# Kernel optimization log

Hardware: AMD Instinct MI355X
Metric: run time of the kernel (lower is better)

Reference implementation:

```python
import jax, jax.numpy as jnp
import numpy as np
import math

STRIDES = [8, 16, 32, 64, 128]
NUM_CLASSES = 80
NUM_ANCHORS = 9
_RATIOS = np.array([0.5, 1.0, 2.0])
_SCALES = 2.0 ** np.array([0.0, 1.0 / 3.0, 2.0 / 3.0])


def _base_anchors(base_size):
    # standard RetinaNet base anchors: 3 ratios x 3 scales, centered at origin
    a = np.zeros((9, 4))
    a[:, 2:] = base_size * np.tile(_SCALES, (2, 3)).T
    areas = a[:, 2] * a[:, 3]
    a[:, 2] = np.sqrt(areas / np.repeat(_RATIOS, 3))
    a[:, 3] = a[:, 2] * np.repeat(_RATIOS, 3)
    a[:, 0::2] -= np.tile(a[:, 2] * 0.5, (2, 1)).T
    a[:, 1::2] -= np.tile(a[:, 3] * 0.5, (2, 1)).T
    return a


def _make_anchors(featmap_sizes):
    per_level = []
    for (h, w), s in zip(featmap_sizes, STRIDES):
        base = _base_anchors(4 * s)  # base_size = 4 * stride (RetinaNet convention)
        sx = (np.arange(w) + 0.5) * s
        sy = (np.arange(h) + 0.5) * s
        X, Y = np.meshgrid(sx, sy)
        shifts = np.stack([X.ravel(), Y.ravel(), X.ravel(), Y.ravel()], axis=1)
        # anchors vary fastest per location -> matches [B,H,W,A,*] flatten order
        per_level.append((shifts[:, None, :] + base[None, :, :]).reshape(-1, 4))
    return jnp.asarray(np.concatenate(per_level, axis=0), dtype=jnp.float32)


def _conv3x3(x, w, b):
    y = jax.lax.conv_general_dilated(x, w, (1, 1), 'SAME', dimension_numbers=('NCHW', 'OIHW', 'NCHW'))
    return y + b[None, :, None, None]


def _tower(x, ws, bs):
    for i in range(4):
        x = jax.nn.relu(_conv3x3(x, ws[i], bs[i]))
    return _conv3x3(x, ws[4], bs[4])


def _bbox_transform(anchors, deltas):
    # BBoxTransform with mean 0, std (0.1, 0.1, 0.2, 0.2)
    w = anchors[:, 2] - anchors[:, 0]
    h = anchors[:, 3] - anchors[:, 1]
    cx = anchors[:, 0] + 0.5 * w
    cy = anchors[:, 1] + 0.5 * h
    pcx = cx + deltas[..., 0] * 0.1 * w
    pcy = cy + deltas[..., 1] * 0.1 * h
    pw = jnp.exp(deltas[..., 2] * 0.2) * w
    ph = jnp.exp(deltas[..., 3] * 0.2) * h
    return jnp.stack([pcx - 0.5 * pw, pcy - 0.5 * ph, pcx + 0.5 * pw, pcy + 0.5 * ph], axis=-1)


def _heads(feats, cls_ws, cls_bs, reg_ws, reg_bs):
    B = feats[0].shape[0]
    cls_l, reg_l = [], []
    for f in feats:
        c = _tower(f, cls_ws, cls_bs)  # [B, 9*80, H, W]
        cls_l.append(jnp.transpose(c, (0, 2, 3, 1)).reshape(B, -1, NUM_CLASSES))
        r = _tower(f, reg_ws, reg_bs)  # [B, 9*4, H, W]
        reg_l.append(jnp.transpose(r, (0, 2, 3, 1)).reshape(B, -1, 4))
    return jnp.concatenate(cls_l, axis=1), jnp.concatenate(reg_l, axis=1)


def setup_inputs():
    key = jax.random.key(0)
    ks = jax.random.split(key, 32)
    B, C = 8, 256
    sizes = [(64, 64), (32, 32), (16, 16), (8, 8), (4, 4)]
    inp = {}
    for i, (h, w) in enumerate(sizes):
        inp['feat%d' % i] = jax.random.normal(ks[i], (B, C, h, w), dtype=jnp.float32)
    prior_bias = -math.log((1.0 - 0.01) / 0.01)

    def mk(k, out_ch, in_ch):
        std = math.sqrt(2.0 / (9.0 * out_ch))  # matches torch init normal_(0, sqrt(2/n))
        return jax.random.normal(k, (out_ch, in_ch, 3, 3), dtype=jnp.float32) * std

    ki = 5
    for i in range(4):
        inp['cls_w%d' % i] = mk(ks[ki], 256, 256); ki += 1
        inp['cls_b%d' % i] = jnp.zeros((256,), jnp.float32)
    inp['cls_w4'] = mk(ks[ki], NUM_ANCHORS * NUM_CLASSES, 256); ki += 1
    inp['cls_b4'] = jnp.full((NUM_ANCHORS * NUM_CLASSES,), prior_bias, jnp.float32)
    for i in range(4):
        inp['reg_w%d' % i] = mk(ks[ki], 256, 256); ki += 1
        inp['reg_b%d' % i] = jnp.zeros((256,), jnp.float32)
    inp['reg_w4'] = mk(ks[ki], NUM_ANCHORS * 4, 256); ki += 1
    inp['reg_b4'] = jnp.full((NUM_ANCHORS * 4,), prior_bias, jnp.float32)
    return inp


def reference(feat0, feat1, feat2, feat3, feat4,
              cls_w0, cls_b0, cls_w1, cls_b1, cls_w2, cls_b2, cls_w3, cls_b3, cls_w4, cls_b4,
              reg_w0, reg_b0, reg_w1, reg_b1, reg_w2, reg_b2, reg_w3, reg_b3, reg_w4, reg_b4):
    feats = [feat0, feat1, feat2, feat3, feat4]
    cls_ws = [cls_w0, cls_w1, cls_w2, cls_w3, cls_w4]
    cls_bs = [cls_b0, cls_b1, cls_b2, cls_b3, cls_b4]
    reg_ws = [reg_w0, reg_w1, reg_w2, reg_w3, reg_w4]
    reg_bs = [reg_b0, reg_b1, reg_b2, reg_b3, reg_b4]
    pred_cls, pred_reg = _heads(feats, cls_ws, cls_bs, reg_ws, reg_bs)
    anchors = _make_anchors([f.shape[-2:] for f in feats])  # [A, 4]
    boxes = _bbox_transform(anchors, pred_reg)  # [B, A, 4]
    probs = jax.nn.sigmoid(pred_cls)  # [B, A, 80]
    scores = jnp.max(probs, axis=2)
    class_id = jnp.argmax(probs, axis=2)
    return scores, class_id, boxes
```

## Files before the change

kernel.cpp:

```cpp
#include <hip/hip_runtime.h>
#include <math.h>

#define CIN 256
#define K9  2304
#define TLW 16
#define TLH 8
#define LIS 22
#define TAU 1e-3f

template<typename TI, typename TA, int CH, bool RELU>
__global__ __launch_bounds__(256, 2) void conv_tile(
    const TI* __restrict__ in, const float* __restrict__ wgt,
    const float* __restrict__ bias, TA* __restrict__ out,
    int H, int W, int C_out)
{
    const int NCH = CIN / CH;
    const int tilesX = (W + TLW - 1) / TLW;
    const int tx = (blockIdx.x % tilesX) * TLW;
    const int ty = (blockIdx.x / tilesX) * TLH;
    const int b  = blockIdx.y;
    const int co0 = blockIdx.z * 64;
    const int tid = threadIdx.x;
    const int tco = (tid >> 5) * 8;
    const int tpx = tid & 31;
    const int prow = tpx >> 2;
    const int pcol = (tpx & 3) * 4;

    __shared__ __align__(16) TA lw[CH * 9 * 64];
    __shared__ __align__(16) TA li[CH * 10 * LIS];

    TA acc[8][4];
    #pragma unroll
    for (int c = 0; c < 8; ++c)
        #pragma unroll
        for (int j = 0; j < 4; ++j) acc[c][j] = (TA)0;

    const int coLim = min(64, C_out - co0);

    for (int ch = 0; ch < NCH; ++ch) {
        const int ci0 = ch * CH;
        for (int idx = tid; idx < CH * 9 * 64; idx += 256) {
            int r  = idx >> 6;
            int co = idx & 63;
            TA v = (TA)0;
            if (co < coLim)
                v = (TA)wgt[(size_t)(co0 + co) * (CIN * 9) + (size_t)ci0 * 9 + r];
            lw[idx] = v;
        }
        for (int idx = tid; idx < CH * 10 * LIS; idx += 256) {
            int ci = idx / (10 * LIS);
            int rr = idx % (10 * LIS);
            int row = rr / LIS, col = rr % LIS;
            TA v = (TA)0;
            int iy = ty + row - 1, ix = tx + col - 1;
            if (col < TLW + 2 && iy >= 0 && iy < H && ix >= 0 && ix < W)
                v = (TA)in[(((size_t)b * CIN + ci0 + ci) * H + iy) * W + ix];
            li[idx] = v;
        }
        __syncthreads();
        #pragma unroll
        for (int ci = 0; ci < CH; ++ci) {
            #pragma unroll
            for (int ky = 0; ky < 3; ++ky) {
                const TA* ip = &li[ci * 10 * LIS + (prow + ky) * LIS + pcol];
                TA ir[6];
                #pragma unroll
                for (int t = 0; t < 6; ++t) ir[t] = ip[t];
                #pragma unroll
                for (int kx = 0; kx < 3; ++kx) {
                    const TA* wp = &lw[(ci * 9 + ky * 3 + kx) * 64 + tco];
                    TA wv[8];
                    #pragma unroll
                    for (int c = 0; c < 8; ++c) wv[c] = wp[c];
                    TA x0 = ir[kx], x1 = ir[kx + 1], x2 = ir[kx + 2], x3 = ir[kx + 3];
                    #pragma unroll
                    for (int c = 0; c < 8; ++c) {
                        acc[c][0] += wv[c] * x0;
                        acc[c][1] += wv[c] * x1;
                        acc[c][2] += wv[c] * x2;
                        acc[c][3] += wv[c] * x3;
                    }
                }
            }
        }
        __syncthreads();
    }

    const int oy = ty + prow;
    if (oy < H) {
        #pragma unroll
        for (int c = 0; c < 8; ++c) {
            int co = co0 + tco + c;
            if (co < C_out) {
                TA bv = (TA)bias[co];
                #pragma unroll
                for (int j = 0; j < 4; ++j) {
                    int ox = tx + pcol + j;
                    if (ox < W) {
                        TA v = acc[c][j] + bv;
                        if (RELU) v = v > (TA)0 ? v : (TA)0;
                        out[(((size_t)b * C_out + co) * H + oy) * W + ox] = v;
                    }
                }
            }
        }
    }
}

#define CH5 8
__global__ __launch_bounds__(256, 2) void cls5_f32(
    const double* __restrict__ in, const float* __restrict__ wgt,
    const float* __restrict__ bias, float* __restrict__ scores,
    float* __restrict__ cls_id, unsigned char* __restrict__ flags,
    int H, int W, int level_off, int A_total, int b0)
{
    const int tilesX = (W + TLW - 1) / TLW;
    const int tx = (blockIdx.x % tilesX) * TLW;
    const int ty = (blockIdx.x / tilesX) * TLH;
    const int b  = blockIdx.y;
    const int a  = blockIdx.z;
    const int co0 = a * 80;
    const int tid = threadIdx.x;
    const int cog = tid >> 5;
    const int tco = cog * 10;
    const int tpx = tid & 31;
    const int prow = tpx >> 2;
    const int pcol = (tpx & 3) * 4;

    __shared__ __align__(16) float lw[CH5 * 9 * 80];
    __shared__ __align__(16) float li[CH5 * 10 * LIS];
    __shared__ float redM1[128 * 8];
    __shared__ float redM2[128 * 8];
    __shared__ int   redA [128 * 8];

    float acc[10][4];
    #pragma unroll
    for (int c = 0; c < 10; ++c)
        #pragma unroll
        for (int j = 0; j < 4; ++j) acc[c][j] = 0.f;

    for (int ch = 0; ch < CIN / CH5; ++ch) {
        const int ci0 = ch * CH5;
        for (int idx = tid; idx < CH5 * 9 * 80; idx += 256) {
            int r  = idx / 80;
            int co = idx % 80;
            lw[idx] = wgt[(size_t)(co0 + co) * (CIN * 9) + (size_t)ci0 * 9 + r];
        }
        for (int idx = tid; idx < CH5 * 10 * LIS; idx += 256) {
            int ci = idx / (10 * LIS);
            int rr = idx % (10 * LIS);
            int row = rr / LIS, col = rr % LIS;
            float v = 0.f;
            int iy = ty + row - 1, ix = tx + col - 1;
            if (col < TLW + 2 && iy >= 0 && iy < H && ix >= 0 && ix < W)
                v = (float)in[(((size_t)b * CIN + ci0 + ci) * H + iy) * W + ix];
            li[idx] = v;
        }
        __syncthreads();
        #pragma unroll
        for (int ci = 0; ci < CH5; ++ci) {
            #pragma unroll
            for (int ky = 0; ky < 3; ++ky) {
                const float* ip = &li[ci * 10 * LIS + (prow + ky) * LIS + pcol];
                float ir[6];
                #pragma unroll
                for (int t = 0; t < 6; ++t) ir[t] = ip[t];
                #pragma unroll
                for (int kx = 0; kx < 3; ++kx) {
                    const float* wp = &lw[(ci * 9 + ky * 3 + kx) * 80 + tco];
                    float wv[10];
                    #pragma unroll
                    for (int c = 0; c < 10; ++c) wv[c] = wp[c];
                    float x0 = ir[kx], x1 = ir[kx + 1], x2 = ir[kx + 2], x3 = ir[kx + 3];
                    #pragma unroll
                    for (int c = 0; c < 10; ++c) {
                        acc[c][0] = fmaf(wv[c], x0, acc[c][0]);
                        acc[c][1] = fmaf(wv[c], x1, acc[c][1]);
                        acc[c][2] = fmaf(wv[c], x2, acc[c][2]);
                        acc[c][3] = fmaf(wv[c], x3, acc[c][3]);
                    }
                }
            }
        }
        __syncthreads();
    }

    #pragma unroll
    for (int j = 0; j < 4; ++j) {
        float m1 = acc[0][j] + bias[co0 + tco];
        float m2 = -3.0e38f;
        int am = tco;
        #pragma unroll
        for (int c = 1; c < 10; ++c) {
            float v = acc[c][j] + bias[co0 + tco + c];
            if (v > m1) { m2 = m1; m1 = v; am = tco + c; }
            else if (v > m2) { m2 = v; }
        }
        int p = prow * 16 + pcol + j;
        redM1[p * 8 + cog] = m1;
        redA [p * 8 + cog] = am;
        redM2[p * 8 + cog] = m2;
    }
    __syncthreads();
    if (tid < 128) {
        int p = tid;
        float m1 = redM1[p * 8]; int am = redA[p * 8]; float m2 = redM2[p * 8];
        #pragma unroll
        for (int t = 1; t < 8; ++t) {
            float rm1 = redM1[p * 8 + t];
            float rm2 = redM2[p * 8 + t];
            if (rm1 > m1) { m2 = fmaxf(m1, rm2); m1 = rm1; am = redA[p * 8 + t]; }
            else          { m2 = fmaxf(m2, rm1); }
        }
        int oy = ty + (p >> 4), ox = tx + (p & 15);
        if (oy < H && ox < W) {
            size_t oi = (size_t)(b0 + b) * A_total + level_off
                      + (size_t)(oy * W + ox) * 9 + a;
            scores[oi] = 1.f / (1.f + expf(-m1));
            cls_id[oi] = (float)am;
            flags[((size_t)b * H * W + oy * W + ox) * 9 + a] =
                (m1 - m2 < TAU) ? 1 : 0;
        }
    }
}

__global__ __launch_bounds__(128) void fixup_cls(
    const double* __restrict__ in, const float* __restrict__ wgt,
    const float* __restrict__ bias, const unsigned char* __restrict__ flags,
    float* __restrict__ scores, float* __restrict__ cls_id,
    int H, int W, int level_off, int A_total, int b0)
{
    const int px = blockIdx.x;
    const int b  = blockIdx.y;
    const int a  = blockIdx.z;
    const int tid = threadIdx.x;
    const unsigned char fl = flags[((size_t)b * H * W + px) * 9 + a];

    __shared__ double patch[K9];
    __shared__ double lg[80];

    if (fl) {
        const int y = px / W, x = px % W;
        for (int idx = tid; idx < K9; idx += 128) {
            int ci = idx / 9, tap = idx % 9;
            int iy = y + tap / 3 - 1, ix = x + tap % 3 - 1;
            double v = 0.0;
            if (iy >= 0 && iy < H && ix >= 0 && ix < W)
                v = in[(((size_t)b * CIN + ci) * H + iy) * W + ix];
            patch[idx] = v;
        }
        __syncthreads();
        if (tid < 80) {
            const float* wr = wgt + (size_t)(a * 80 + tid) * K9;
            double s = 0.0;
            for (int k = 0; k < K9; ++k) s += (double)wr[k] * patch[k];
            lg[tid] = s + (double)bias[a * 80 + tid];
        }
        __syncthreads();
        if (tid == 0) {
            double m = lg[0]; int am = 0;
            for (int c = 1; c < 80; ++c)
                if (lg[c] > m) { m = lg[c]; am = c; }
            size_t oi = (size_t)(b0 + b) * A_total + level_off + (size_t)px * 9 + a;
            scores[oi] = (float)(1.0 / (1.0 + exp(-m)));
            cls_id[oi] = (float)am;
        }
    }
}

__global__ void boxes_ep(const float* __restrict__ reg5, float* __restrict__ boxes,
                         int H, int W, int level_off, int A_total, float stride,
                         int b0, int Bc)
{
    int idx = blockIdx.x * 256 + threadIdx.x;
    int total = Bc * H * W * 9;
    if (idx >= total) return;
    int a = idx % 9; int rest = idx / 9;
    int x = rest % W; rest /= W;
    int y = rest % H; int b = rest / H;

    float base = 4.f * stride;
    float scale = exp2f((float)(a % 3) * (1.f / 3.f));
    int ri = a / 3;
    float sr = (ri == 0) ? 0.70710678118654752f : (ri == 1 ? 1.f : 1.41421356237309505f);
    float wa = base * scale / sr;
    float ha = base * scale * sr;
    float cx = (x + 0.5f) * stride, cy = (y + 0.5f) * stride;

    size_t cs = (size_t)H * W;
    const float* rp = reg5 + (((size_t)b * 36 + a * 4) * H + y) * W + x;
    float d0 = rp[0], d1 = rp[cs], d2 = rp[2 * cs], d3 = rp[3 * cs];

    float pcx = cx + d0 * 0.1f * wa;
    float pcy = cy + d1 * 0.1f * ha;
    float pw  = expf(d2 * 0.2f) * wa;
    float ph  = expf(d3 * 0.2f) * ha;

    size_t oi = ((size_t)(b0 + b) * A_total + level_off
               + (size_t)(y * W + x) * 9 + a) * 4;
    boxes[oi + 0] = pcx - 0.5f * pw;
    boxes[oi + 1] = pcy - 0.5f * ph;
    boxes[oi + 2] = pcx + 0.5f * pw;
    boxes[oi + 3] = pcy + 0.5f * ph;
}

extern "C" void kernel_launch(void* const* d_in, const int* in_sizes, int n_in,
                              void* d_out, int out_size, void* d_ws, size_t ws_size,
                              hipStream_t stream)
{
    const float* feats[5];
    for (int i = 0; i < 5; ++i) feats[i] = (const float*)d_in[i];
    const float* cw[5]; const float* cb[5];
    const float* rw[5]; const float* rb[5];
    for (int i = 0; i < 5; ++i) {
        cw[i] = (const float*)d_in[5 + 2 * i];
        cb[i] = (const float*)d_in[6 + 2 * i];
        rw[i] = (const float*)d_in[15 + 2 * i];
        rb[i] = (const float*)d_in[16 + 2 * i];
    }

    const int A_total = 49104;
    float* scores = (float*)d_out;
    float* cls_id = scores + (size_t)8 * A_total;
    float* boxes  = scores + (size_t)2 * 8 * A_total;

    const int   Hs[5]      = {64, 32, 16, 8, 4};
    const float strides[5] = {8.f, 16.f, 32.f, 64.f, 128.f};
    const int   offs[5]    = {0, 36864, 46080, 48384, 48960};

    const size_t flagRes = 131072;
    unsigned char* flags = (unsigned char*)d_ws;
    char*  actBase  = (char*)d_ws + flagRes;
    size_t actBytes = ws_size > flagRes ? ws_size - flagRes : 0;

    for (int l = 0; l < 5; ++l) {
        int H = Hs[l], W = Hs[l];
        size_t perb = (size_t)CIN * H * W;
        int Bc = 8;
        while (Bc > 1 && 2ull * Bc * perb * 8 > actBytes) Bc >>= 1;
        double* D0 = (double*)actBase;
        double* D1 = D0 + (size_t)Bc * perb;
        int tiles = ((W + TLW - 1) / TLW) * ((H + TLH - 1) / TLH);
        for (int b0 = 0; b0 < 8; b0 += Bc) {
            const float* fin = feats[l] + (size_t)b0 * perb;
            dim3 g(tiles, Bc, 4);
            conv_tile<float,  double, 8, true><<<g, 256, 0, stream>>>(fin, cw[0], cb[0], D0, H, W, 256);
            conv_tile<double, double, 8, true><<<g, 256, 0, stream>>>(D0,  cw[1], cb[1], D1, H, W, 256);
            conv_tile<double, double, 8, true><<<g, 256, 0, stream>>>(D1,  cw[2], cb[2], D0, H, W, 256);
            conv_tile<double, double, 8, true><<<g, 256, 0, stream>>>(D0,  cw[3], cb[3], D1, H, W, 256);
            dim3 g5(tiles, Bc, 9);
            cls5_f32<<<g5, 256, 0, stream>>>(D1, cw[4], cb[4], scores, cls_id,
                                             flags, H, W, offs[l], A_total, b0);
            dim3 gf(H * W, Bc, 9);
            fixup_cls<<<gf, 128, 0, stream>>>(D1, cw[4], cb[4], flags,
                                              scores, cls_id,
                                              H, W, offs[l], A_total, b0);
        }
    }

    for (int l = 0; l < 5; ++l) {
        int H = Hs[l], W = Hs[l];
        size_t perb = (size_t)CIN * H * W;
        int Br = 8;
        while (Br > 1 && 2ull * Br * perb * 4 > actBytes) Br >>= 1;
        float* F0 = (float*)actBase;
        float* F1 = F0 + (size_t)Br * perb;
        int tiles = ((W + TLW - 1) / TLW) * ((H + TLH - 1) / TLH);
        for (int b0 = 0; b0 < 8; b0 += Br) {
            dim3 g(tiles, Br, 4);
            const float* fin = feats[l] + (size_t)b0 * perb;
            conv_tile<float, float, 8, true><<<g, 256, 0, stream>>>(fin, rw[0], rb[0], F0, H, W, 256);
            conv_tile<float, float, 8, true><<<g, 256, 0, stream>>>(F0,  rw[1], rb[1], F1, H, W, 256);
            conv_tile<float, float, 8, true><<<g, 256, 0, stream>>>(F1,  rw[2], rb[2], F0, H, W, 256);
            conv_tile<float, float, 8, true><<<g, 256, 0, stream>>>(F0,  rw[3], rb[3], F1, H, W, 256);
            dim3 gr(tiles, Br, 1);
            conv_tile<float, float, 8, false><<<gr, 256, 0, stream>>>(F1, rw[4], rb[4], F0, H, W, 36);
            int total = Br * H * W * 9;
            boxes_ep<<<(total + 255) / 256, 256, 0, stream>>>(F0, boxes, H, W,
                                                              offs[l], A_total,
                                                              strides[l], b0, Br);
        }
    }
}
```

Measured before the change: 24.80 ms.

## Unfuse final cls conv from argmax epilogue; reuse generic conv tile

Replaces the specialized fused final classification conv (conv plus per-tile max/argmax reduction through shared memory) with the generic conv_tile kernel writing the 720-channel logits to a float workspace. A separate elementwise epilogue kernel then computes the top-2, sigmoid score, class id and tie flag per anchor. This drops the shared-memory reduction and the 10-channel-per-thread register layout of the fused kernel in favour of the generic conv's 64-channel blocking. In exchange it adds a logits round trip through global memory and shrinks the batch chunk to fit the extra buffer.

```diff
diff --git a/kernel.cpp b/kernel.cpp
--- a/kernel.cpp
+++ b/kernel.cpp
@@ -107,120 +107,27 @@
     }
 }
 
-#define CH5 8
-__global__ __launch_bounds__(256, 2) void cls5_f32(
-    const double* __restrict__ in, const float* __restrict__ wgt,
-    const float* __restrict__ bias, float* __restrict__ scores,
+__global__ __launch_bounds__(256) void cls_ep(
+    const float* __restrict__ lg, float* __restrict__ scores,
     float* __restrict__ cls_id, unsigned char* __restrict__ flags,
-    int H, int W, int level_off, int A_total, int b0)
-{
-    const int tilesX = (W + TLW - 1) / TLW;
-    const int tx = (blockIdx.x % tilesX) * TLW;
-    const int ty = (blockIdx.x / tilesX) * TLH;
-    const int b  = blockIdx.y;
-    const int a  = blockIdx.z;
-    const int co0 = a * 80;
-    const int tid = threadIdx.x;
-    const int cog = tid >> 5;
-    const int tco = cog * 10;
-    const int tpx = tid & 31;
-    const int prow = tpx >> 2;
-    const int pcol = (tpx & 3) * 4;
-
-    __shared__ __align__(16) float lw[CH5 * 9 * 80];
-    __shared__ __align__(16) float li[CH5 * 10 * LIS];
-    __shared__ float redM1[128 * 8];
-    __shared__ float redM2[128 * 8];
-    __shared__ int   redA [128 * 8];
-
-    float acc[10][4];
-    #pragma unroll
-    for (int c = 0; c < 10; ++c)
-        #pragma unroll
-        for (int j = 0; j < 4; ++j) acc[c][j] = 0.f;
-
-    for (int ch = 0; ch < CIN / CH5; ++ch) {
-        const int ci0 = ch * CH5;
-        for (int idx = tid; idx < CH5 * 9 * 80; idx += 256) {
-            int r  = idx / 80;
-            int co = idx % 80;
-            lw[idx] = wgt[(size_t)(co0 + co) * (CIN * 9) + (size_t)ci0 * 9 + r];
-        }
-        for (int idx = tid; idx < CH5 * 10 * LIS; idx += 256) {
-            int ci = idx / (10 * LIS);
-            int rr = idx % (10 * LIS);
-            int row = rr / LIS, col = rr % LIS;
-            float v = 0.f;
-            int iy = ty + row - 1, ix = tx + col - 1;
-            if (col < TLW + 2 && iy >= 0 && iy < H && ix >= 0 && ix < W)
-                v = (float)in[(((size_t)b * CIN + ci0 + ci) * H + iy) * W + ix];
-            li[idx] = v;
-        }
-        __syncthreads();
-        #pragma unroll
-        for (int ci = 0; ci < CH5; ++ci) {
-            #pragma unroll
-            for (int ky = 0; ky < 3; ++ky) {
-                const float* ip = &li[ci * 10 * LIS + (prow + ky) * LIS + pcol];
-                float ir[6];
-                #pragma unroll
-                for (int t = 0; t < 6; ++t) ir[t] = ip[t];
-                #pragma unroll
-                for (int kx = 0; kx < 3; ++kx) {
-                    const float* wp = &lw[(ci * 9 + ky * 3 + kx) * 80 + tco];
-                    float wv[10];
-                    #pragma unroll
-                    for (int c = 0; c < 10; ++c) wv[c] = wp[c];
-                    float x0 = ir[kx], x1 = ir[kx + 1], x2 = ir[kx + 2], x3 = ir[kx + 3];
-                    #pragma unroll
-                    for (int c = 0; c < 10; ++c) {
-                        acc[c][0] = fmaf(wv[c], x0, acc[c][0]);
-                        acc[c][1] = fmaf(wv[c], x1, acc[c][1]);
-                        acc[c][2] = fmaf(wv[c], x2, acc[c][2]);
-                        acc[c][3] = fmaf(wv[c], x3, acc[c][3]);
-                    }
-                }
-            }
-        }
-        __syncthreads();
-    }
-
-    #pragma unroll
-    for (int j = 0; j < 4; ++j) {
-        float m1 = acc[0][j] + bias[co0 + tco];
-        float m2 = -3.0e38f;
-        int am = tco;
-        #pragma unroll
-        for (int c = 1; c < 10; ++c) {
-            float v = acc[c][j] + bias[co0 + tco + c];
-            if (v > m1) { m2 = m1; m1 = v; am = tco + c; }
+    int HW, int level_off, int A_total, int b0, int Bc)
+{
+    int idx = blockIdx.x * 256 + threadIdx.x;
+    if (idx >= Bc * HW) return;
+    int b = idx / HW, px = idx % HW;
+    const float* base = lg + (size_t)b * 720 * HW + px;
+    for (int a = 0; a < 9; ++a) {
+        float m1 = -3.0e38f, m2 = -3.0e38f;
+        int am = 0;
+        for (int c = 0; c < 80; ++c) {
+            float v = base[(size_t)(a * 80 + c) * HW];
+            if (v > m1) { m2 = m1; m1 = v; am = c; }
             else if (v > m2) { m2 = v; }
         }
-        int p = prow * 16 + pcol + j;
-        redM1[p * 8 + cog] = m1;
-        redA [p * 8 + cog] = am;
-        redM2[p * 8 + cog] = m2;
-    }
-    __syncthreads();
-    if (tid < 128) {
-        int p = tid;
-        float m1 = redM1[p * 8]; int am = redA[p * 8]; float m2 = redM2[p * 8];
-        #pragma unroll
-        for (int t = 1; t < 8; ++t) {
-            float rm1 = redM1[p * 8 + t];
-            float rm2 = redM2[p * 8 + t];
-            if (rm1 > m1) { m2 = fmaxf(m1, rm2); m1 = rm1; am = redA[p * 8 + t]; }
-            else          { m2 = fmaxf(m2, rm1); }
-        }
-        int oy = ty + (p >> 4), ox = tx + (p & 15);
-        if (oy < H && ox < W) {
-            size_t oi = (size_t)(b0 + b) * A_total + level_off
-                      + (size_t)(oy * W + ox) * 9 + a;
-            scores[oi] = 1.f / (1.f + expf(-m1));
-            cls_id[oi] = (float)am;
-            flags[((size_t)b * H * W + oy * W + ox) * 9 + a] =
-                (m1 - m2 < TAU) ? 1 : 0;
-        }
+        size_t oi = (size_t)(b0 + b) * A_total + level_off + (size_t)px * 9 + a;
+        scores[oi] = 1.f / (1.f + expf(-m1));
+        cls_id[oi] = (float)am;
+        flags[((size_t)b * HW + px) * 9 + a] = (m1 - m2 < TAU) ? 1 : 0;
     }
 }
 
@@ -335,11 +242,14 @@
 
     for (int l = 0; l < 5; ++l) {
         int H = Hs[l], W = Hs[l];
-        size_t perb = (size_t)CIN * H * W;
+        int HW = H * W;
+        size_t perb = (size_t)CIN * HW;
         int Bc = 8;
-        while (Bc > 1 && 2ull * Bc * perb * 8 > actBytes) Bc >>= 1;
+        while (Bc > 1 &&
+               (size_t)Bc * (16ull * perb + 2880ull * HW) > actBytes) Bc >>= 1;
         double* D0 = (double*)actBase;
         double* D1 = D0 + (size_t)Bc * perb;
+        float*  LG = (float*)(D1 + (size_t)Bc * perb);
         int tiles = ((W + TLW - 1) / TLW) * ((H + TLH - 1) / TLH);
         for (int b0 = 0; b0 < 8; b0 += Bc) {
             const float* fin = feats[l] + (size_t)b0 * perb;
@@ -348,10 +258,12 @@
             conv_tile<double, double, 8, true><<<g, 256, 0, stream>>>(D0,  cw[1], cb[1], D1, H, W, 256);
             conv_tile<double, double, 8, true><<<g, 256, 0, stream>>>(D1,  cw[2], cb[2], D0, H, W, 256);
             conv_tile<double, double, 8, true><<<g, 256, 0, stream>>>(D0,  cw[3], cb[3], D1, H, W, 256);
-            dim3 g5(tiles, Bc, 9);
-            cls5_f32<<<g5, 256, 0, stream>>>(D1, cw[4], cb[4], scores, cls_id,
-                                             flags, H, W, offs[l], A_total, b0);
-            dim3 gf(H * W, Bc, 9);
+            dim3 g5(tiles, Bc, 12);
+            conv_tile<double, float, 8, false><<<g5, 256, 0, stream>>>(
+                D1, cw[4], cb[4], LG, H, W, 720);
+            cls_ep<<<(Bc * HW + 255) / 256, 256, 0, stream>>>(
+                LG, scores, cls_id, flags, HW, offs[l], A_total, b0, Bc);
+            dim3 gf(HW, Bc, 9);
             fixup_cls<<<gf, 128, 0, stream>>>(D1, cw[4], cb[4], flags,
                                               scores, cls_id,
                                               H, W, offs[l], A_total, b0);
```

Measured after the change: 25.01 ms. Within noise of the previous version (+0.9%).
